# Kernel optimization log

Hardware: AMD Instinct MI355X
Metric: run time of the kernel (lower is better)

## Reference

```python
import jax, jax.numpy as jnp
import numpy as np

E = 250000   # n_scanned_edges
B = 16       # batch_size
N = 50000    # n_entities (n_nodes)
R = 500      # n_relations
D_IN = 100   # input embedding dim (proj input)
D = 64       # n_dims_sm
M = 2 * E    # n_memorized_and_scanned_nodes (>= n_vi_groups + n_vj_groups)


def setup_inputs() -> dict:
    rng = np.random.default_rng(0)
    eg = rng.integers(0, B, E)
    vi = rng.integers(0, N, E)
    vj = rng.integers(0, N, E)
    order = np.lexsort((vj, vi, eg))  # sorted by (eg_idx, vi, vj) as the module assumes
    eg, vi, vj = eg[order], vi[order], vj[order]
    rel = rng.integers(0, R, E)
    # dense group ids; idx_vi is non-decreasing because edges are lexsorted by (eg,vi)
    idx_vi = np.unique(eg.astype(np.int64) * N + vi, return_inverse=True)[1]
    idx_vj = np.unique(eg.astype(np.int64) * N + vj, return_inverse=True)[1]
    n_vi = int(idx_vi.max()) + 1
    edges = np.stack([eg, vi, vj, rel, idx_vi, idx_vj, idx_vi, n_vi + idx_vj], 1).astype(np.int32)

    key = jax.random.key(0)
    ks = jax.random.split(key, 24)
    nrm = lambda k, shp, s=1.0: jax.random.normal(k, shp, jnp.float32) * s
    na = jax.random.uniform(ks[0], (B, N), jnp.float32)
    na = na / jnp.sum(na, 1, keepdims=True)  # node attention is a distribution per example
    inp = {
        "node_attention": na,
        "scanned_edges": jnp.asarray(edges),
        "hidden_uncon": nrm(ks[1], (1, N, D_IN)),
        "hidden_con": nrm(ks[2], (M, D_IN)),
        "rel_table": nrm(ks[3], (R, D_IN)),
        "query_head_emb": nrm(ks[4], (B, D_IN)),
        "query_rel_emb": nrm(ks[5], (B, D_IN)),
        "p_W": nrm(ks[6], (D_IN, D), 0.1),
        "p_b": jnp.zeros((D,), jnp.float32),
    }
    i = 7
    for g in ("g1", "g2"):
        for nm, shp in (("lW", (4 * D, D)), ("lb", (D,)), ("rW", (4 * D, D)), ("rb", (D,)), ("cW", (D, D)), ("cb", (D,))):
            inp[g + "_" + nm] = nrm(ks[i], shp, 0.05)
            i += 1
    return inp


def _g(left, right, lW, lb, rW, rb, cW, cb):
    # G layer: sum(left_dense(cat(left)) * center_dense(right_dense(cat(right))), -1)
    lx = jnp.concatenate(left, -1)
    rx = jnp.concatenate(right, -1)
    l = jax.nn.leaky_relu(lx @ lW + lb, 0.2)  # tf.nn.leaky_relu alpha=0.2
    r = jax.nn.leaky_relu(rx @ rW + rb, 0.2)
    return jnp.sum(l * (r @ cW + cb), -1)


def reference(node_attention, scanned_edges, hidden_uncon, hidden_con, rel_table,
              query_head_emb, query_rel_emb, p_W, p_b,
              g1_lW, g1_lb, g1_rW, g1_rb, g1_cW, g1_cb,
              g2_lW, g2_lb, g2_rW, g2_rb, g2_cW, g2_cb):
    Bn, Nn = node_attention.shape
    En = scanned_edges.shape[0]
    proj = lambda x: jnp.tanh(x @ p_W + p_b)

    h_con = proj(hidden_con)       # (M, D)
    h_uncon = proj(hidden_uncon)   # (1, N, D)
    qh = proj(query_head_emb)      # (B, D)
    qr = proj(query_rel_emb)

    e = scanned_edges
    eg, vi, vj = e[:, 0], e[:, 1], e[:, 2]
    idx_vi = e[:, 4]
    # node2edge gathers
    h_vi = h_con[e[:, 6]]          # (E, D)
    h_vj = h_con[e[:, 7]]
    hu_vj = h_uncon[0][vj]         # hidden_uncon batch is 1 -> idx 0
    remb = proj(rel_table[e[:, 3]])
    qhv = qh[eg]
    qrv = qr[eg]

    left = (h_vi, remb, qhv, qrv)
    logits = _g(left, (h_vj, remb, qhv, qrv), g1_lW, g1_lb, g1_rW, g1_rb, g1_cW, g1_cb)
    logits = logits + _g(left, (hu_vj, remb, qhv, qrv), g2_lW, g2_lb, g2_rW, g2_rb, g2_cW, g2_cb)

    # neighbor softmax over sorted idx_vi segments
    m = jax.ops.segment_max(logits, idx_vi, num_segments=En, indices_are_sorted=True)
    ex = jnp.exp(logits - m[idx_vi])
    den = jax.ops.segment_sum(ex, idx_vi, num_segments=En, indices_are_sorted=True)
    transition = ex / den[idx_vi]

    # flow attention: gather at (eg, vi), scatter-sum at (eg, vj)
    trans_att = node_attention[eg, vi] * transition
    new_att = jnp.zeros((Bn, Nn), node_attention.dtype).at[eg, vj].add(trans_att)
    new_att = new_att / jnp.sum(new_att, axis=1, keepdims=True)
    return new_att
```

## Files before the change

### kernel.cpp

```cpp
#include <hip/hip_runtime.h>

#define DIN 100
#define DD  64
#define NE  250000
#define NB  16
#define NN  50000
#define NR  500
#define NM  500000
#define NH  (NM + NN)

#define H_OFF    64
#define TA2_OFF  (H_OFF + NH*DD)
#define RT_OFF   (TA2_OFF + NE*DD)
#define QT_OFF   (RT_OFF + 4*NR*DD)
#define LG_OFF   (QT_OFF + 4*NB*DD)

#define PA 480
#define PB 240
#define PC 48

__device__ __forceinline__ void fma4x4(const float4 x, const float4 w, float4 acc[4]) {
  acc[0].x += x.x*w.x; acc[0].y += x.x*w.y; acc[0].z += x.x*w.z; acc[0].w += x.x*w.w;
  acc[1].x += x.y*w.x; acc[1].y += x.y*w.y; acc[1].z += x.y*w.z; acc[1].w += x.y*w.w;
  acc[2].x += x.z*w.x; acc[2].y += x.z*w.y; acc[2].z += x.z*w.z; acc[2].w += x.z*w.w;
  acc[3].x += x.w*w.x; acc[3].y += x.w*w.y; acc[3].z += x.w*w.z; acc[3].w += x.w*w.w;
}

__device__ __forceinline__ float4 leaky4(float4 v) {
  v.x = v.x > 0.f ? v.x : 0.2f*v.x;
  v.y = v.y > 0.f ? v.y : 0.2f*v.y;
  v.z = v.z > 0.f ? v.z : 0.2f*v.z;
  v.w = v.w > 0.f ? v.w : 0.2f*v.w;
  return v;
}

__global__ void k_init(int* wsI, float* bsum) {
  if (threadIdx.x == 0) { wsI[0] = 0x7fffffff; wsI[1] = 0; }
  if (threadIdx.x < NB) bsum[threadIdx.x] = 0.f;
}

__global__ void k_limits(const int* __restrict__ edges, int* __restrict__ wsI) {
  int i = blockIdx.x * blockDim.x + threadIdx.x;
  int mn = 0x7fffffff, mx = -1;
  if (i < NE) { int v = edges[i*8 + 7]; mn = v; mx = v; }
  for (int off = 32; off > 0; off >>= 1) {
    mn = min(mn, __shfl_down(mn, off));
    mx = max(mx, __shfl_down(mx, off));
  }
  if ((threadIdx.x & 63) == 0) {
    atomicMin(&wsI[0], mn);
    atomicMax(&wsI[1], mx + 1);
  }
}

__global__ void k_tables(const float* __restrict__ rtab,
                         const float* __restrict__ qh, const float* __restrict__ qr,
                         const float* __restrict__ pW, const float* __restrict__ pb,
                         const float* __restrict__ g1_lW, const float* __restrict__ g1_lb,
                         const float* __restrict__ g1_rW, const float* __restrict__ g1_rb,
                         const float* __restrict__ g2_lW, const float* __restrict__ g2_lb,
                         const float* __restrict__ g2_rW, const float* __restrict__ g2_rb,
                         float* __restrict__ rT, float* __restrict__ qT) {
  __shared__ float xs[DIN], xs2[DIN], ps[DD], ps2[DD];
  const int d = threadIdx.x;
  const int blk = blockIdx.x;
  if (blk < NR) {
    for (int k = d; k < DIN; k += 64) xs[k] = rtab[blk*DIN + k];
    __syncthreads();
    float a = pb[d];
    for (int k = 0; k < DIN; ++k) a += xs[k] * pW[k*DD + d];
    ps[d] = tanhf(a);
    __syncthreads();
    float o1 = 0.f, o2 = 0.f, o3 = 0.f, o4 = 0.f;
    for (int k = 0; k < DD; ++k) {
      float p = ps[k];
      o1 += p * g1_lW[(DD + k)*DD + d];
      o2 += p * g1_rW[(DD + k)*DD + d];
      o3 += p * g2_lW[(DD + k)*DD + d];
      o4 += p * g2_rW[(DD + k)*DD + d];
    }
    rT[(0*NR + blk)*DD + d] = o1;
    rT[(1*NR + blk)*DD + d] = o2;
    rT[(2*NR + blk)*DD + d] = o3;
    rT[(3*NR + blk)*DD + d] = o4;
  } else {
    const int b = blk - NR;
    for (int k = d; k < DIN; k += 64) { xs[k] = qh[b*DIN + k]; xs2[k] = qr[b*DIN + k]; }
    __syncthreads();
    float a = pb[d], a2 = pb[d];
    for (int k = 0; k < DIN; ++k) { a += xs[k]*pW[k*DD + d]; a2 += xs2[k]*pW[k*DD + d]; }
    ps[d] = tanhf(a); ps2[d] = tanhf(a2);
    __syncthreads();
    float o1 = g1_lb[d], o2 = g1_rb[d], o3 = g2_lb[d], o4 = g2_rb[d];
    for (int k = 0; k < DD; ++k) {
      float p = ps[k], p2 = ps2[k];
      o1 += p * g1_lW[(2*DD + k)*DD + d] + p2 * g1_lW[(3*DD + k)*DD + d];
      o2 += p * g1_rW[(2*DD + k)*DD + d] + p2 * g1_rW[(3*DD + k)*DD + d];
      o3 += p * g2_lW[(2*DD + k)*DD + d] + p2 * g2_lW[(3*DD + k)*DD + d];
      o4 += p * g2_rW[(2*DD + k)*DD + d] + p2 * g2_rW[(3*DD + k)*DD + d];
    }
    qT[(0*NB + b)*DD + d] = o1;
    qT[(1*NB + b)*DD + d] = o2;
    qT[(2*NB + b)*DD + d] = o3;
    qT[(3*NB + b)*DD + d] = o4;
  }
}

__global__ __launch_bounds__(256, 3)
void k_proj(const float* __restrict__ hcon, const float* __restrict__ huncon,
            const float* __restrict__ pW, const float* __restrict__ pb,
            const int* __restrict__ lim, float* __restrict__ H) {
  __shared__ __align__(16) float pWs[DIN*DD];
  __shared__ __align__(16) float Xt[DIN][68];
  const int tid = threadIdx.x;
  for (int i = tid; i < DIN*DD; i += 256) pWs[i] = pW[i];
  const int c0 = (tid & 15) << 2;
  const int r0 = (tid >> 4) << 2;
  const float4 pbv = *(const float4*)&pb[c0];
  const int nmax = lim[1];
  const int t_lo = (nmax + 63) >> 6;
  const int NT   = t_lo + (NN + 63) / 64;
  __syncthreads();
  for (int t = blockIdx.x; t < NT; t += gridDim.x) {
    const int row0 = (t < t_lo) ? t*64 : NM + (t - t_lo)*64;
    for (int i = tid; i < 64*DIN; i += 256) {
      int r = i / DIN, k = i - r*DIN;
      int row = row0 + r;
      float v = 0.f;
      if (row < NH) v = (row < NM) ? hcon[row*DIN + k] : huncon[(row - NM)*DIN + k];
      Xt[k][r] = v;
    }
    __syncthreads();
    float4 acc[4] = {{0,0,0,0},{0,0,0,0},{0,0,0,0},{0,0,0,0}};
    for (int k = 0; k < DIN; ++k) {
      float4 x = *(const float4*)&Xt[k][r0];
      float4 w = *(const float4*)&pWs[k*DD + c0];
      fma4x4(x, w, acc);
    }
    #pragma unroll
    for (int i = 0; i < 4; ++i) {
      int row = row0 + r0 + i;
      if (row < NH) {
        float4 o;
        o.x = tanhf(acc[i].x + pbv.x);
        o.y = tanhf(acc[i].y + pbv.y);
        o.z = tanhf(acc[i].z + pbv.z);
        o.w = tanhf(acc[i].w + pbv.w);
        *(float4*)&H[row*DD + c0] = o;
      }
    }
    __syncthreads();
  }
}

__global__ __launch_bounds__(256, 3)
void k_tf(const float* __restrict__ g1_lW, const float* __restrict__ g1_rW,
          const float* __restrict__ g2_lW, const float* __restrict__ g2_rW,
          const int* __restrict__ lim,
          float* __restrict__ H, float* __restrict__ TA2) {
  __shared__ __align__(16) float Ws0[DD*DD];
  __shared__ __align__(16) float Ws1[DD*DD];
  __shared__ __align__(16) float Ht[DD][68];
  const int tid = threadIdx.x;
  const int nvi  = lim[0];
  const int nmax = lim[1];
  int pool, pbase, pgrid;
  if (blockIdx.x < PA)           { pool = 0; pbase = blockIdx.x;           pgrid = PA; }
  else if (blockIdx.x < PA + PB) { pool = 1; pbase = blockIdx.x - PA;      pgrid = PB; }
  else                           { pool = 2; pbase = blockIdx.x - PA - PB; pgrid = PC; }
  if (pool == 0) {
    for (int i = tid; i < DD*DD; i += 256) { Ws0[i] = g1_lW[i]; Ws1[i] = g2_lW[i]; }
  } else if (pool == 1) {
    for (int i = tid; i < DD*DD; i += 256) Ws0[i] = g1_rW[i];
  } else {
    for (int i = tid; i < DD*DD; i += 256) Ws0[i] = g2_rW[i];
  }
  int t_begin, t_count, row_base;
  if (pool == 0)      { t_begin = 0;        t_count = (nvi + 63) >> 6;                 row_base = 0;  }
  else if (pool == 1) { t_begin = nvi >> 6; t_count = ((nmax + 63) >> 6) - (nvi >> 6); row_base = 0;  }
  else                { t_begin = 0;        t_count = (NN + 63) >> 6;                  row_base = NM; }
  const int c0 = (tid & 15) << 2;
  const int r0 = (tid >> 4) << 2;
  __syncthreads();
  for (int tt = pbase; tt < t_count; tt += pgrid) {
    const int row0 = row_base + (t_begin + tt)*64;
    for (int i = tid; i < 64*DD; i += 256) {
      int d = i & 63, r = i >> 6;
      int row = row0 + r;
      Ht[d][r] = (row < NH) ? H[row*DD + d] : 0.f;
    }
    __syncthreads();
    float4 a0[4] = {{0,0,0,0},{0,0,0,0},{0,0,0,0},{0,0,0,0}};
    for (int k = 0; k < DD; ++k) {
      float4 x = *(const float4*)&Ht[k][r0];
      float4 w = *(const float4*)&Ws0[k*DD + c0];
      fma4x4(x, w, a0);
    }
    if (pool == 0) {
      float4 a1[4] = {{0,0,0,0},{0,0,0,0},{0,0,0,0},{0,0,0,0}};
      for (int k = 0; k < DD; ++k) {
        float4 x = *(const float4*)&Ht[k][r0];
        float4 w = *(const float4*)&Ws1[k*DD + c0];
        fma4x4(x, w, a1);
      }
      #pragma unroll
      for (int i = 0; i < 4; ++i) {
        int row = row0 + r0 + i;
        if (row < nvi) {
          *(float4*)&H[row*DD + c0]   = a0[i];
          *(float4*)&TA2[row*DD + c0] = a1[i];
        }
      }
    } else if (pool == 1) {
      #pragma unroll
      for (int i = 0; i < 4; ++i) {
        int row = row0 + r0 + i;
        if (row >= nvi && row < nmax) *(float4*)&H[row*DD + c0] = a0[i];
      }
    } else {
      #pragma unroll
      for (int i = 0; i < 4; ++i) {
        int row = row0 + r0 + i;
        if (row < NH) *(float4*)&H[row*DD + c0] = a0[i];
      }
    }
    __syncthreads();
  }
}

__global__ __launch_bounds__(256, 2)
void k_edges(const int* __restrict__ edges,
             const float* __restrict__ TA, const float* __restrict__ TA2,
             const float* __restrict__ HU2,
             const float* __restrict__ rT, const float* __restrict__ qT,
             const float* __restrict__ cW1, const float* __restrict__ cb1,
             const float* __restrict__ cW2, const float* __restrict__ cb2,
             float* __restrict__ logits) {
  __shared__ __align__(16) float Wt1s[DD*68];
  __shared__ __align__(16) float Wt2s[DD*68];
  __shared__ __align__(16) float Lt[DD][68];
  __shared__ __align__(16) float Rt[DD][68];
  __shared__ __align__(16) float4 cbs4[2][16];
  __shared__ float lg[64];
  __shared__ int   se[64*8];
  const int tid = threadIdx.x;
  for (int i = tid; i < DD*DD; i += 256) {
    int k = i >> 6, d = i & 63;
    Wt1s[d*68 + k] = cW1[i];
    Wt2s[d*68 + k] = cW2[i];
  }
  if (tid < 16) {
    cbs4[0][tid] = *(const float4*)&cb1[tid*4];
    cbs4[1][tid] = *(const float4*)&cb2[tid*4];
  }
  const int e   = tid >> 2;
  const int d0  = (tid & 3) * 16;
  const int ee0 = (tid & 15) << 2;
  const int k0  = (tid >> 4) << 2;
  __syncthreads();
  const int NT = (NE + 63) / 64;
  for (int tile = blockIdx.x; tile < NT; tile += gridDim.x) {
    const int e0 = tile * 64;
    const int ecnt = min(64, NE - e0);
    for (int i = tid; i < 64*8; i += 256) se[i] = (i < ecnt*8) ? edges[e0*8 + i] : 0;
    if (tid < 64) lg[tid] = 0.f;
    __syncthreads();
    const int rel = se[e*8 + 3];
    const int eg  = se[e*8 + 0];
    const int li  = se[e*8 + 6];
    for (int g = 0; g < 2; ++g) {
      const float* Lb = g ? TA2 : TA;
      const float* Rb = g ? HU2 : TA;
      const float* rL = rT + (g ? 2*NR*DD : 0);
      const float* rR = rT + (g ? 3*NR*DD : 1*NR*DD);
      const float* qL = qT + (g ? 2*NB*DD : 0);
      const float* qR = qT + (g ? 3*NB*DD : 1*NB*DD);
      const float* Wts = g ? Wt2s : Wt1s;
      const int ri = g ? se[e*8 + 2] : se[e*8 + 7];
      float cbp = 0.f;
      #pragma unroll
      for (int di = 0; di < 4; ++di) {
        const int d = d0 + 4*di;
        float4 l = *(const float4*)&Lb[li*DD + d];
        float4 t = *(const float4*)&rL[rel*DD + d];
        float4 u = *(const float4*)&qL[eg*DD + d];
        l.x += t.x + u.x; l.y += t.y + u.y; l.z += t.z + u.z; l.w += t.w + u.w;
        l = leaky4(l);
        Lt[d+0][e] = l.x; Lt[d+1][e] = l.y; Lt[d+2][e] = l.z; Lt[d+3][e] = l.w;
        float4 c = cbs4[g][d >> 2];
        cbp += l.x*c.x + l.y*c.y + l.z*c.z + l.w*c.w;
        float4 r = *(const float4*)&Rb[ri*DD + d];
        t = *(const float4*)&rR[rel*DD + d];
        u = *(const float4*)&qR[eg*DD + d];
        r.x += t.x + u.x; r.y += t.y + u.y; r.z += t.z + u.z; r.w += t.w + u.w;
        r = leaky4(r);
        Rt[d+0][e] = r.x; Rt[d+1][e] = r.y; Rt[d+2][e] = r.z; Rt[d+3][e] = r.w;
      }
      atomicAdd(&lg[e], cbp);
      __syncthreads();
      float4 z[4] = {{0,0,0,0},{0,0,0,0},{0,0,0,0},{0,0,0,0}};
      for (int d = 0; d < DD; ++d) {
        float4 x = *(const float4*)&Lt[d][ee0];
        float4 w = *(const float4*)&Wts[d*68 + k0];
        fma4x4(x, w, z);
      }
      {
        float4 r0v = *(const float4*)&Rt[k0+0][ee0];
        float4 r1v = *(const float4*)&Rt[k0+1][ee0];
        float4 r2v = *(const float4*)&Rt[k0+2][ee0];
        float4 r3v = *(const float4*)&Rt[k0+3][ee0];
        float p0 = z[0].x*r0v.x + z[0].y*r1v.x + z[0].z*r2v.x + z[0].w*r3v.x;
        float p1 = z[1].x*r0v.y + z[1].y*r1v.y + z[1].z*r2v.y + z[1].w*r3v.y;
        float p2 = z[2].x*r0v.z + z[2].y*r1v.z + z[2].z*r2v.z + z[2].w*r3v.z;
        float p3 = z[3].x*r0v.w + z[3].y*r1v.w + z[3].z*r2v.w + z[3].w*r3v.w;
        atomicAdd(&lg[ee0+0], p0);
        atomicAdd(&lg[ee0+1], p1);
        atomicAdd(&lg[ee0+2], p2);
        atomicAdd(&lg[ee0+3], p3);
      }
      __syncthreads();
    }
    if (tid < ecnt) logits[e0 + tid] = lg[tid];
    __syncthreads();
  }
}

__global__ void k_softmax(const int* __restrict__ edges, const float* __restrict__ logits,
                          const float* __restrict__ na, float* __restrict__ out) {
  int e = blockIdx.x * blockDim.x + threadIdx.x;
  if (e >= NE) return;
  int seg = edges[e*8 + 4];
  if (e > 0 && edges[(e-1)*8 + 4] == seg) return;
  int j = e;
  float m = -1e30f;
  while (j < NE && edges[j*8 + 4] == seg) { m = fmaxf(m, logits[j]); ++j; }
  float s = 0.f;
  for (int t = e; t < j; ++t) s += expf(logits[t] - m);
  int eg = edges[e*8 + 0], vi = edges[e*8 + 1];
  float scale = na[eg*NN + vi] / s;
  for (int t = e; t < j; ++t) {
    int vj = edges[t*8 + 2];
    __hip_atomic_fetch_add(&out[eg*NN + vj], expf(logits[t] - m) * scale,
                           __ATOMIC_RELAXED, __HIP_MEMORY_SCOPE_AGENT);
  }
}

__global__ void k_rowsum(const float* __restrict__ out, float* __restrict__ bsum) {
  int b = blockIdx.y;
  float s = 0.f;
  for (int n = blockIdx.x * blockDim.x + threadIdx.x; n < NN; n += gridDim.x * blockDim.x)
    s += out[b*NN + n];
  for (int off = 32; off > 0; off >>= 1) s += __shfl_down(s, off);
  if ((threadIdx.x & 63) == 0)
    __hip_atomic_fetch_add(&bsum[b], s, __ATOMIC_RELAXED, __HIP_MEMORY_SCOPE_AGENT);
}

__global__ void k_div(float* __restrict__ out, const float* __restrict__ bsum) {
  int i = blockIdx.x * blockDim.x + threadIdx.x;
  if (i < NB*NN) out[i] /= bsum[i / NN];
}

extern "C" void kernel_launch(void* const* d_in, const int* in_sizes, int n_in,
                              void* d_out, int out_size, void* d_ws, size_t ws_size,
                              hipStream_t stream) {
  (void)in_sizes; (void)n_in; (void)out_size; (void)ws_size;
  const float* na     = (const float*)d_in[0];
  const int*   edges  = (const int*)  d_in[1];
  const float* huncon = (const float*)d_in[2];
  const float* hcon   = (const float*)d_in[3];
  const float* rtab   = (const float*)d_in[4];
  const float* qh     = (const float*)d_in[5];
  const float* qr     = (const float*)d_in[6];
  const float* pW     = (const float*)d_in[7];
  const float* pb     = (const float*)d_in[8];
  const float* g1_lW  = (const float*)d_in[9];
  const float* g1_lb  = (const float*)d_in[10];
  const float* g1_rW  = (const float*)d_in[11];
  const float* g1_rb  = (const float*)d_in[12];
  const float* g1_cW  = (const float*)d_in[13];
  const float* g1_cb  = (const float*)d_in[14];
  const float* g2_lW  = (const float*)d_in[15];
  const float* g2_lb  = (const float*)d_in[16];
  const float* g2_rW  = (const float*)d_in[17];
  const float* g2_rb  = (const float*)d_in[18];
  const float* g2_cW  = (const float*)d_in[19];
  const float* g2_cb  = (const float*)d_in[20];
  float* out  = (float*)d_out;
  float* ws   = (float*)d_ws;
  int*   wsI  = (int*)d_ws;
  float* bsum = ws + 16;
  float* H    = ws + H_OFF;
  float* TA2  = ws + TA2_OFF;
  float* rT   = ws + RT_OFF;
  float* qT   = ws + QT_OFF;
  float* lgp  = ws + LG_OFF;

  hipMemsetAsync(d_out, 0, (size_t)NB*NN*sizeof(float), stream);
  k_init<<<1, 64, 0, stream>>>(wsI, bsum);
  k_limits<<<(NE + 255)/256, 256, 0, stream>>>(edges, wsI);
  k_tables<<<NR + NB, 64, 0, stream>>>(rtab, qh, qr, pW, pb,
                                       g1_lW, g1_lb, g1_rW, g1_rb,
                                       g2_lW, g2_lb, g2_rW, g2_rb, rT, qT);
  k_proj<<<768, 256, 0, stream>>>(hcon, huncon, pW, pb, wsI, H);
  k_tf<<<PA + PB + PC, 256, 0, stream>>>(g1_lW, g1_rW, g2_lW, g2_rW, wsI, H, TA2);
  k_edges<<<512, 256, 0, stream>>>(edges, H, TA2, H + NM*DD, rT, qT,
                                   g1_cW, g1_cb, g2_cW, g2_cb, lgp);
  k_softmax<<<(NE + 255)/256, 256, 0, stream>>>(edges, lgp, na, out);
  k_rowsum<<<dim3(32, 16), 256, 0, stream>>>(out, bsum);
  k_div<<<(NB*NN + 255)/256, 256, 0, stream>>>(out, bsum);
}
```

Baseline: 967.0 us.

## Use 256-row tiles with 8x8 register blocking in projection and transform GEMMs

k_proj and k_tf now process 256-row tiles instead of 64, with each thread computing an 8x8 output block instead of 4x4. Each thread loads its own input row with float4 reads and scatters it transposed into shared memory, in K-chunks to fit the larger tile. The goal is more FMAs per shared-memory load, fewer scattered global loads and fewer tile iterations. The cost is higher register pressure (launch bounds drop to 2 blocks per SM), grid sizes reduced to match, and strided transposed shared-memory writes that may cause bank conflicts.

```diff
diff --git a/kernel.cpp b/kernel.cpp
--- a/kernel.cpp
+++ b/kernel.cpp
@@ -15,9 +15,11 @@
 #define QT_OFF   (RT_OFF + 4*NR*DD)
 #define LG_OFF   (QT_OFF + 4*NB*DD)
 
-#define PA 480
-#define PB 240
-#define PC 48
+#define PA 320
+#define PB 160
+#define PC 32
+
+#define XT_STRIDE 260
 
 __device__ __forceinline__ void fma4x4(const float4 x, const float4 w, float4 acc[4]) {
   acc[0].x += x.x*w.x; acc[0].y += x.x*w.y; acc[0].z += x.x*w.z; acc[0].w += x.x*w.w;
@@ -106,61 +108,85 @@
   }
 }
 
-__global__ __launch_bounds__(256, 3)
+__global__ __launch_bounds__(256, 2)
 void k_proj(const float* __restrict__ hcon, const float* __restrict__ huncon,
             const float* __restrict__ pW, const float* __restrict__ pb,
             const int* __restrict__ lim, float* __restrict__ H) {
   __shared__ __align__(16) float pWs[DIN*DD];
-  __shared__ __align__(16) float Xt[DIN][68];
+  __shared__ __align__(16) float Xt[52][XT_STRIDE];
   const int tid = threadIdx.x;
   for (int i = tid; i < DIN*DD; i += 256) pWs[i] = pW[i];
-  const int c0 = (tid & 15) << 2;
-  const int r0 = (tid >> 4) << 2;
-  const float4 pbv = *(const float4*)&pb[c0];
+  const int tc = tid & 7, tr = tid >> 3;
+  const int c0 = tc << 3;
+  const float4 pb0 = *(const float4*)&pb[c0];
+  const float4 pb1 = *(const float4*)&pb[c0 + 4];
   const int nmax = lim[1];
-  const int t_lo = (nmax + 63) >> 6;
-  const int NT   = t_lo + (NN + 63) / 64;
+  const int t_lo = (nmax + 255) >> 8;
+  const int NT   = t_lo + ((NN + 255) >> 8);
   __syncthreads();
   for (int t = blockIdx.x; t < NT; t += gridDim.x) {
-    const int row0 = (t < t_lo) ? t*64 : NM + (t - t_lo)*64;
-    for (int i = tid; i < 64*DIN; i += 256) {
-      int r = i / DIN, k = i - r*DIN;
-      int row = row0 + r;
-      float v = 0.f;
-      if (row < NH) v = (row < NM) ? hcon[row*DIN + k] : huncon[(row - NM)*DIN + k];
-      Xt[k][r] = v;
+    const int row0 = (t < t_lo) ? (t << 8) : (NM + ((t - t_lo) << 8));
+    const int myrow = row0 + tid;
+    const float* src = nullptr;
+    if (myrow < NH) src = (myrow < NM) ? &hcon[myrow*DIN] : &huncon[(myrow - NM)*DIN];
+    float4 acc[2][2][4];
+    #pragma unroll
+    for (int a = 0; a < 2; ++a)
+      #pragma unroll
+      for (int b = 0; b < 2; ++b)
+        #pragma unroll
+        for (int i = 0; i < 4; ++i) acc[a][b][i] = make_float4(0.f,0.f,0.f,0.f);
+    #pragma unroll
+    for (int chunk = 0; chunk < 2; ++chunk) {
+      const int kb = chunk ? 48 : 0;
+      const int klen = chunk ? 52 : 48;
+      __syncthreads();
+      if (src) {
+        for (int j = 0; j < klen; j += 4) {
+          float4 v = *(const float4*)&src[kb + j];
+          Xt[j+0][tid] = v.x; Xt[j+1][tid] = v.y; Xt[j+2][tid] = v.z; Xt[j+3][tid] = v.w;
+        }
+      }
+      __syncthreads();
+      for (int k = 0; k < klen; ++k) {
+        float4 x0 = *(const float4*)&Xt[k][tr*8];
+        float4 x1 = *(const float4*)&Xt[k][tr*8 + 4];
+        float4 w0 = *(const float4*)&pWs[(kb + k)*DD + c0];
+        float4 w1 = *(const float4*)&pWs[(kb + k)*DD + c0 + 4];
+        fma4x4(x0, w0, acc[0][0]); fma4x4(x0, w1, acc[0][1]);
+        fma4x4(x1, w0, acc[1][0]); fma4x4(x1, w1, acc[1][1]);
+      }
     }
-    __syncthreads();
-    float4 acc[4] = {{0,0,0,0},{0,0,0,0},{0,0,0,0},{0,0,0,0}};
-    for (int k = 0; k < DIN; ++k) {
-      float4 x = *(const float4*)&Xt[k][r0];
-      float4 w = *(const float4*)&pWs[k*DD + c0];
-      fma4x4(x, w, acc);
-    }
-    #pragma unroll
-    for (int i = 0; i < 4; ++i) {
-      int row = row0 + r0 + i;
-      if (row < NH) {
-        float4 o;
-        o.x = tanhf(acc[i].x + pbv.x);
-        o.y = tanhf(acc[i].y + pbv.y);
-        o.z = tanhf(acc[i].z + pbv.z);
-        o.w = tanhf(acc[i].w + pbv.w);
-        *(float4*)&H[row*DD + c0] = o;
-      }
-    }
-    __syncthreads();
-  }
-}
-
-__global__ __launch_bounds__(256, 3)
+    #pragma unroll
+    for (int a = 0; a < 2; ++a)
+      #pragma unroll
+      for (int i = 0; i < 4; ++i) {
+        int row = row0 + tr*8 + a*4 + i;
+        if (row < NH) {
+          float4 o0, o1;
+          o0.x = tanhf(acc[a][0][i].x + pb0.x);
+          o0.y = tanhf(acc[a][0][i].y + pb0.y);
+          o0.z = tanhf(acc[a][0][i].z + pb0.z);
+          o0.w = tanhf(acc[a][0][i].w + pb0.w);
+          o1.x = tanhf(acc[a][1][i].x + pb1.x);
+          o1.y = tanhf(acc[a][1][i].y + pb1.y);
+          o1.z = tanhf(acc[a][1][i].z + pb1.z);
+          o1.w = tanhf(acc[a][1][i].w + pb1.w);
+          *(float4*)&H[row*DD + c0]     = o0;
+          *(float4*)&H[row*DD + c0 + 4] = o1;
+        }
+      }
+  }
+}
+
+__global__ __launch_bounds__(256, 2)
 void k_tf(const float* __restrict__ g1_lW, const float* __restrict__ g1_rW,
           const float* __restrict__ g2_lW, const float* __restrict__ g2_rW,
           const int* __restrict__ lim,
           float* __restrict__ H, float* __restrict__ TA2) {
   __shared__ __align__(16) float Ws0[DD*DD];
   __shared__ __align__(16) float Ws1[DD*DD];
-  __shared__ __align__(16) float Ht[DD][68];
+  __shared__ __align__(16) float Ht[32][XT_STRIDE];
   const int tid = threadIdx.x;
   const int nvi  = lim[0];
   const int nmax = lim[1];
@@ -176,55 +202,80 @@
     for (int i = tid; i < DD*DD; i += 256) Ws0[i] = g2_rW[i];
   }
   int t_begin, t_count, row_base;
-  if (pool == 0)      { t_begin = 0;        t_count = (nvi + 63) >> 6;                 row_base = 0;  }
-  else if (pool == 1) { t_begin = nvi >> 6; t_count = ((nmax + 63) >> 6) - (nvi >> 6); row_base = 0;  }
-  else                { t_begin = 0;        t_count = (NN + 63) >> 6;                  row_base = NM; }
-  const int c0 = (tid & 15) << 2;
-  const int r0 = (tid >> 4) << 2;
+  if (pool == 0)      { t_begin = 0;        t_count = (nvi + 255) >> 8;                 row_base = 0;  }
+  else if (pool == 1) { t_begin = nvi >> 8; t_count = ((nmax + 255) >> 8) - (nvi >> 8); row_base = 0;  }
+  else                { t_begin = 0;        t_count = (NN + 255) >> 8;                  row_base = NM; }
+  const int tc = tid & 7, tr = tid >> 3;
+  const int c0 = tc << 3;
   __syncthreads();
   for (int tt = pbase; tt < t_count; tt += pgrid) {
-    const int row0 = row_base + (t_begin + tt)*64;
-    for (int i = tid; i < 64*DD; i += 256) {
-      int d = i & 63, r = i >> 6;
-      int row = row0 + r;
-      Ht[d][r] = (row < NH) ? H[row*DD + d] : 0.f;
+    const int row0 = row_base + ((t_begin + tt) << 8);
+    const int myrow = row0 + tid;
+    float4 a0[2][2][4], a1[2][2][4];
+    #pragma unroll
+    for (int a = 0; a < 2; ++a)
+      #pragma unroll
+      for (int b = 0; b < 2; ++b)
+        #pragma unroll
+        for (int i = 0; i < 4; ++i) {
+          a0[a][b][i] = make_float4(0.f,0.f,0.f,0.f);
+          a1[a][b][i] = make_float4(0.f,0.f,0.f,0.f);
+        }
+    #pragma unroll
+    for (int chunk = 0; chunk < 2; ++chunk) {
+      const int kb = chunk << 5;
+      __syncthreads();
+      if (myrow < NH) {
+        const float* src = &H[myrow*DD + kb];
+        #pragma unroll
+        for (int j = 0; j < 32; j += 4) {
+          float4 v = *(const float4*)&src[j];
+          Ht[j+0][tid] = v.x; Ht[j+1][tid] = v.y; Ht[j+2][tid] = v.z; Ht[j+3][tid] = v.w;
+        }
+      }
+      __syncthreads();
+      if (pool == 0) {
+        for (int k = 0; k < 32; ++k) {
+          float4 x0 = *(const float4*)&Ht[k][tr*8];
+          float4 x1 = *(const float4*)&Ht[k][tr*8 + 4];
+          float4 w0 = *(const float4*)&Ws0[(kb + k)*DD + c0];
+          float4 w1 = *(const float4*)&Ws0[(kb + k)*DD + c0 + 4];
+          float4 u0 = *(const float4*)&Ws1[(kb + k)*DD + c0];
+          float4 u1 = *(const float4*)&Ws1[(kb + k)*DD + c0 + 4];
+          fma4x4(x0, w0, a0[0][0]); fma4x4(x0, w1, a0[0][1]);
+          fma4x4(x1, w0, a0[1][0]); fma4x4(x1, w1, a0[1][1]);
+          fma4x4(x0, u0, a1[0][0]); fma4x4(x0, u1, a1[0][1]);
+          fma4x4(x1, u0, a1[1][0]); fma4x4(x1, u1, a1[1][1]);
+        }
+      } else {
+        for (int k = 0; k < 32; ++k) {
+          float4 x0 = *(const float4*)&Ht[k][tr*8];
+          float4 x1 = *(const float4*)&Ht[k][tr*8 + 4];
+          float4 w0 = *(const float4*)&Ws0[(kb + k)*DD + c0];
+          float4 w1 = *(const float4*)&Ws0[(kb + k)*DD + c0 + 4];
+          fma4x4(x0, w0, a0[0][0]); fma4x4(x0, w1, a0[0][1]);
+          fma4x4(x1, w0, a0[1][0]); fma4x4(x1, w1, a0[1][1]);
+        }
+      }
     }
-    __syncthreads();
-    float4 a0[4] = {{0,0,0,0},{0,0,0,0},{0,0,0,0},{0,0,0,0}};
-    for (int k = 0; k < DD; ++k) {
-      float4 x = *(const float4*)&Ht[k][r0];
-      float4 w = *(const float4*)&Ws0[k*DD + c0];
-      fma4x4(x, w, a0);
-    }
-    if (pool == 0) {
-      float4 a1[4] = {{0,0,0,0},{0,0,0,0},{0,0,0,0},{0,0,0,0}};
-      for (int k = 0; k < DD; ++k) {
-        float4 x = *(const float4*)&Ht[k][r0];
-        float4 w = *(const float4*)&Ws1[k*DD + c0];
-        fma4x4(x, w, a1);
-      }
+    #pragma unroll
+    for (int a = 0; a < 2; ++a)
       #pragma unroll
       for (int i = 0; i < 4; ++i) {
-        int row = row0 + r0 + i;
-        if (row < nvi) {
-          *(float4*)&H[row*DD + c0]   = a0[i];
-          *(float4*)&TA2[row*DD + c0] = a1[i];
-        }
-      }
-    } else if (pool == 1) {
-      #pragma unroll
-      for (int i = 0; i < 4; ++i) {
-        int row = row0 + r0 + i;
-        if (row >= nvi && row < nmax) *(float4*)&H[row*DD + c0] = a0[i];
-      }
-    } else {
-      #pragma unroll
-      for (int i = 0; i < 4; ++i) {
-        int row = row0 + r0 + i;
-        if (row < NH) *(float4*)&H[row*DD + c0] = a0[i];
-      }
-    }
-    __syncthreads();
+        int row = row0 + tr*8 + a*4 + i;
+        bool ok;
+        if (pool == 0)      ok = (row < nvi);
+        else if (pool == 1) ok = (row >= nvi && row < nmax);
+        else                ok = (row < NH);
+        if (ok) {
+          *(float4*)&H[row*DD + c0]     = a0[a][0][i];
+          *(float4*)&H[row*DD + c0 + 4] = a0[a][1][i];
+          if (pool == 0) {
+            *(float4*)&TA2[row*DD + c0]     = a1[a][0][i];
+            *(float4*)&TA2[row*DD + c0 + 4] = a1[a][1][i];
+          }
+        }
+      }
   }
 }
 
@@ -401,7 +452,7 @@
   k_tables<<<NR + NB, 64, 0, stream>>>(rtab, qh, qr, pW, pb,
                                        g1_lW, g1_lb, g1_rW, g1_rb,
                                        g2_lW, g2_lb, g2_rW, g2_rb, rT, qT);
-  k_proj<<<768, 256, 0, stream>>>(hcon, huncon, pW, pb, wsI, H);
+  k_proj<<<512, 256, 0, stream>>>(hcon, huncon, pW, pb, wsI, H);
   k_tf<<<PA + PB + PC, 256, 0, stream>>>(g1_lW, g1_rW, g2_lW, g2_rW, wsI, H, TA2);
   k_edges<<<512, 256, 0, stream>>>(edges, H, TA2, H + NM*DD, rT, qT,
                                    g1_cW, g1_cb, g2_cW, g2_cb, lgp);
```

Result: faster. 816.8 us (-15.5%).
